# Optimization experiments

Hardware: AMD Instinct MI355X
Metric: run time of the kernel (lower is better)

The kernel has to match this reference:

```python
import jax, jax.numpy as jnp
import numpy as np

N, E, D, H, O = 10000, 640000, 128, 256, 1


def setup_inputs() -> dict:
    key = jax.random.key(0)
    ks = jax.random.split(key, 10)
    s = 0.05
    return {
        "x": jax.random.normal(ks[0], (N, D), dtype=jnp.float32),
        "edge_index": jax.random.randint(ks[1], (2, E), 0, N, dtype=jnp.int64),
        # GraphConv (PyG): lin_rel (with bias) applied to sum-aggregated neighbors,
        # lin_root (no bias) applied to self features.
        "W_rel": jax.random.normal(ks[2], (D, D), dtype=jnp.float32) * s,
        "b_rel": jnp.zeros((D,), dtype=jnp.float32),
        "W_root": jax.random.normal(ks[3], (D, D), dtype=jnp.float32) * s,
        # MLP: D -> H -> H -> O, ReLU between layers
        "W1": jax.random.normal(ks[4], (H, D), dtype=jnp.float32) * s,
        "b1": jnp.zeros((H,), dtype=jnp.float32),
        "W2": jax.random.normal(ks[5], (H, H), dtype=jnp.float32) * s,
        "b2": jnp.zeros((H,), dtype=jnp.float32),
        "W3": jax.random.normal(ks[6], (O, H), dtype=jnp.float32) * s,
        "b3": jnp.zeros((O,), dtype=jnp.float32),
    }


def reference(x, edge_index, W_rel, b_rel, W_root, W1, b1, W2, b2, W3, b3):
    src, dst = edge_index[0], edge_index[1]
    # gather source features along edges, scatter-add to destinations
    agg = jax.ops.segment_sum(x[src], dst, num_segments=N)  # [N, D]
    h = agg @ W_rel.T + b_rel + x @ W_root.T                 # GraphConv out [N, D]
    h = jax.nn.relu(h @ W1.T + b1)
    h = jax.nn.relu(h @ W2.T + b2)
    h = h @ W3.T + b3                                        # [N, O]
    return jax.nn.sigmoid(h)
```

## Files before the change

kernel.cpp:

```cpp
#include <hip/hip_runtime.h>
#include <hip/hip_bf16.h>
#include <cmath>

constexpr int N_NODES = 10000;
constexpr int D_IN = 128;
constexpr int H_DIM = 256;

constexpr int NB = 157;
constexpr int BCAP = 8192;
constexpr int EPB_A = 4096;

typedef unsigned short u16;
typedef short bf16x8 __attribute__((ext_vector_type(8)));
typedef float f32x4 __attribute__((ext_vector_type(4)));

__device__ inline u16 f2bf(float f) {
    return __builtin_bit_cast(u16, __float2bfloat16(f));
}
__device__ inline float bf2f(u16 u) {
    unsigned int v = (unsigned int)u << 16;
    return __builtin_bit_cast(float, v);
}

constexpr int PREP_XB = 1250, PREP_WB = 128;
__global__ __launch_bounds__(256)
void prep_kernel(const float* __restrict__ x,
                 const float* __restrict__ W_rel, const float* __restrict__ W_root,
                 const float* __restrict__ W1, const float* __restrict__ W2,
                 u16* __restrict__ x_bf,
                 u16* __restrict__ Wcat, u16* __restrict__ W1b, u16* __restrict__ W2b,
                 int* __restrict__ gcnt) {
    const int bid = blockIdx.x, t = threadIdx.x;
    if (bid < PREP_XB) {
        int idx = bid * 256 + t;
        if (idx >= N_NODES * 32) return;
        int row = idx >> 5, c = (idx & 31) * 4;
        float4 v = *reinterpret_cast<const float4*>(x + (size_t)row * D_IN + c);
        ushort4 o;
        o.x = f2bf(v.x); o.y = f2bf(v.y); o.z = f2bf(v.z); o.w = f2bf(v.w);
        *reinterpret_cast<ushort4*>(x_bf + (size_t)row * D_IN + c) = o;
    } else if (bid < PREP_XB + PREP_WB) {
        int idx4 = ((bid - PREP_XB) * 256 + t) * 4;
        const float* src;
        u16* dst;
        if (idx4 < 32768) {
            int n = idx4 >> 8, k = idx4 & 255;
            src = (k < 128) ? W_rel + n * 128 + k : W_root + n * 128 + (k - 128);
            dst = Wcat + idx4;
        } else if (idx4 < 65536) {
            src = W1 + (idx4 - 32768);
            dst = W1b + (idx4 - 32768);
        } else {
            src = W2 + (idx4 - 65536);
            dst = W2b + (idx4 - 65536);
        }
        float4 v = *reinterpret_cast<const float4*>(src);
        ushort4 o;
        o.x = f2bf(v.x); o.y = f2bf(v.y); o.z = f2bf(v.z); o.w = f2bf(v.w);
        *reinterpret_cast<ushort4*>(dst) = o;
    } else {
        if (t < NB) gcnt[t] = 0;
    }
}

__global__ __launch_bounds__(256)
void binsort_a(const int* __restrict__ ei, int* __restrict__ gcnt,
               int* __restrict__ buckets, int E) {
    __shared__ int lcnt[NB], gbase[NB];
    const int t = threadIdx.x;
    for (int i = t; i < NB; i += 256) lcnt[i] = 0;
    __syncthreads();
    const int e0 = blockIdx.x * EPB_A + t;
    int packed[16], lpos[16], bb[16];
#pragma unroll
    for (int j = 0; j < 16; ++j) {
        int e = e0 + j * 256;
        if (e < E) {
            int s = ei[e], d = ei[E + e];
            int b = d >> 6;
            bb[j] = b;
            packed[j] = ((d & 63) << 16) | s;
            lpos[j] = atomicAdd(&lcnt[b], 1);
        } else bb[j] = -1;
    }
    __syncthreads();
    for (int i = t; i < NB; i += 256)
        gbase[i] = atomicAdd(&gcnt[i], lcnt[i]);
    __syncthreads();
#pragma unroll
    for (int j = 0; j < 16; ++j)
        if (bb[j] >= 0)
            buckets[bb[j] * BCAP + gbase[bb[j]] + lpos[j]] = packed[j];
}

__global__ __launch_bounds__(512)
void mega_kernel(const int* __restrict__ gcnt, const int* __restrict__ buckets,
                 const u16* __restrict__ x_bf,
                 const u16* __restrict__ Wcat, const u16* __restrict__ W1b,
                 const u16* __restrict__ W2b,
                 const float* __restrict__ b_rel, const float* __restrict__ b1,
                 const float* __restrict__ b2, const float* __restrict__ W3,
                 const float* __restrict__ b3, float* __restrict__ out, int M) {
    __shared__ int edges[BCAP];
    __shared__ u16 ssrc[BCAP];
    __shared__ u16 bufA[64 * 264];
    __shared__ u16 bufH0[64 * 136];
    __shared__ int deg[64], cur[64], sbeg[64];
    __shared__ float part[64][4];
    const int b = blockIdx.x, t = threadIdx.x;
    const int w = t >> 6, lane = t & 63;
    const int wm = w >> 2, wn = w & 3;
    const int l16 = lane & 15, q = lane >> 4;
    const int r0 = b * 64;

    if (t < 64) deg[t] = 0;
    __syncthreads();
    int cnt = gcnt[b]; if (cnt > BCAP) cnt = BCAP;
    for (int i = t; i < cnt; i += 512) {
        int p = buckets[b * BCAP + i];
        edges[i] = p;
        atomicAdd(&deg[p >> 16], 1);
    }
    __syncthreads();
    if (t < 64) {
        int d = deg[t];
        int incl = d;
#pragma unroll
        for (int off = 1; off < 64; off <<= 1) {
            int o = __shfl_up(incl, off);
            if (t >= off) incl += o;
        }
        int excl = incl - d;
        cur[t] = excl;
        sbeg[t] = excl;
    }
    __syncthreads();
    for (int i = t; i < cnt; i += 512) {
        int p = edges[i];
        int pos = atomicAdd(&cur[p >> 16], 1);
        ssrc[pos] = (u16)(p & 0xffff);
    }
    for (int idx = t; idx < 64 * 16; idx += 512) {
        int row = idx >> 4, kc = (idx & 15) * 8;
        int gr = r0 + row; if (gr >= M) gr = M - 1;
        bf16x8 v = *reinterpret_cast<const bf16x8*>(x_bf + (size_t)gr * D_IN + kc);
        *reinterpret_cast<bf16x8*>(&bufA[row * 264 + 128 + kc]) = v;
    }
    __syncthreads();
    {
        const int c = (lane & 31) * 4;
        const int r = lane >> 5;
        for (int j = 0; j < 8; ++j) {
            int ln = w * 8 + j;
            int beg = sbeg[ln], dg = deg[ln];
            int half = (dg + 1) >> 1;
            int i = beg + (r ? half : 0);
            const int i1 = r ? beg + dg : beg + half;
            float4 a0 = {0, 0, 0, 0}, a1 = {0, 0, 0, 0};
            float4 a2 = {0, 0, 0, 0}, a3 = {0, 0, 0, 0};
            for (; i + 4 <= i1; i += 4) {
                int s0 = ssrc[i + 0], s1 = ssrc[i + 1];
                int s2 = ssrc[i + 2], s3 = ssrc[i + 3];
                ushort4 v0 = *reinterpret_cast<const ushort4*>(x_bf + (size_t)s0 * D_IN + c);
                ushort4 v1 = *reinterpret_cast<const ushort4*>(x_bf + (size_t)s1 * D_IN + c);
                ushort4 v2 = *reinterpret_cast<const ushort4*>(x_bf + (size_t)s2 * D_IN + c);
                ushort4 v3 = *reinterpret_cast<const ushort4*>(x_bf + (size_t)s3 * D_IN + c);
                a0.x += bf2f(v0.x); a0.y += bf2f(v0.y); a0.z += bf2f(v0.z); a0.w += bf2f(v0.w);
                a1.x += bf2f(v1.x); a1.y += bf2f(v1.y); a1.z += bf2f(v1.z); a1.w += bf2f(v1.w);
                a2.x += bf2f(v2.x); a2.y += bf2f(v2.y); a2.z += bf2f(v2.z); a2.w += bf2f(v2.w);
                a3.x += bf2f(v3.x); a3.y += bf2f(v3.y); a3.z += bf2f(v3.z); a3.w += bf2f(v3.w);
            }
            for (; i < i1; ++i) {
                int s = ssrc[i];
                ushort4 v = *reinterpret_cast<const ushort4*>(x_bf + (size_t)s * D_IN + c);
                a0.x += bf2f(v.x); a0.y += bf2f(v.y); a0.z += bf2f(v.z); a0.w += bf2f(v.w);
            }
            a0.x += a1.x + a2.x + a3.x;
            a0.y += a1.y + a2.y + a3.y;
            a0.z += a1.z + a2.z + a3.z;
            a0.w += a1.w + a2.w + a3.w;
            a0.x += __shfl_xor(a0.x, 32);
            a0.y += __shfl_xor(a0.y, 32);
            a0.z += __shfl_xor(a0.z, 32);
            a0.w += __shfl_xor(a0.w, 32);
            if (r == 0) {
                ushort4 o;
                o.x = f2bf(a0.x); o.y = f2bf(a0.y); o.z = f2bf(a0.z); o.w = f2bf(a0.w);
                *reinterpret_cast<ushort4*>(&bufA[ln * 264 + c]) = o;
            }
        }
    }
    __syncthreads();

    {
        f32x4 acc[2][2] = {};
#pragma unroll
        for (int k0 = 0; k0 < 256; k0 += 32) {
            bf16x8 af[2];
#pragma unroll
            for (int i = 0; i < 2; ++i)
                af[i] = *reinterpret_cast<const bf16x8*>(
                    &bufA[(wm * 32 + i * 16 + l16) * 264 + k0 + q * 8]);
#pragma unroll
            for (int jj = 0; jj < 2; ++jj) {
                int col = wn * 32 + jj * 16 + l16;
                bf16x8 bv = *reinterpret_cast<const bf16x8*>(
                    Wcat + (size_t)col * 256 + k0 + q * 8);
                acc[0][jj] = __builtin_amdgcn_mfma_f32_16x16x32_bf16(af[0], bv, acc[0][jj], 0, 0, 0);
                acc[1][jj] = __builtin_amdgcn_mfma_f32_16x16x32_bf16(af[1], bv, acc[1][jj], 0, 0, 0);
            }
        }
#pragma unroll
        for (int i = 0; i < 2; ++i)
#pragma unroll
            for (int jj = 0; jj < 2; ++jj) {
                int col = wn * 32 + jj * 16 + l16;
                float bb = b_rel[col];
#pragma unroll
                for (int r = 0; r < 4; ++r) {
                    int row = wm * 32 + i * 16 + q * 4 + r;
                    bufH0[row * 136 + col] = f2bf(acc[i][jj][r] + bb);
                }
            }
    }
    __syncthreads();

    {
        f32x4 acc[2][4] = {};
#pragma unroll
        for (int k0 = 0; k0 < 128; k0 += 32) {
            bf16x8 af[2];
#pragma unroll
            for (int i = 0; i < 2; ++i)
                af[i] = *reinterpret_cast<const bf16x8*>(
                    &bufH0[(wm * 32 + i * 16 + l16) * 136 + k0 + q * 8]);
#pragma unroll
            for (int jj = 0; jj < 4; ++jj) {
                int col = wn * 64 + jj * 16 + l16;
                bf16x8 bv = *reinterpret_cast<const bf16x8*>(
                    W1b + (size_t)col * 128 + k0 + q * 8);
                acc[0][jj] = __builtin_amdgcn_mfma_f32_16x16x32_bf16(af[0], bv, acc[0][jj], 0, 0, 0);
                acc[1][jj] = __builtin_amdgcn_mfma_f32_16x16x32_bf16(af[1], bv, acc[1][jj], 0, 0, 0);
            }
        }
        __syncthreads();
#pragma unroll
        for (int i = 0; i < 2; ++i)
#pragma unroll
            for (int jj = 0; jj < 4; ++jj) {
                int col = wn * 64 + jj * 16 + l16;
                float bb = b1[col];
#pragma unroll
                for (int r = 0; r < 4; ++r) {
                    int row = wm * 32 + i * 16 + q * 4 + r;
                    bufA[row * 264 + col] = f2bf(fmaxf(acc[i][jj][r] + bb, 0.f));
                }
            }
    }
    __syncthreads();

    {
        f32x4 acc[2][4] = {};
#pragma unroll
        for (int k0 = 0; k0 < 256; k0 += 32) {
            bf16x8 af[2];
#pragma unroll
            for (int i = 0; i < 2; ++i)
                af[i] = *reinterpret_cast<const bf16x8*>(
                    &bufA[(wm * 32 + i * 16 + l16) * 264 + k0 + q * 8]);
#pragma unroll
            for (int jj = 0; jj < 4; ++jj) {
                int col = wn * 64 + jj * 16 + l16;
                bf16x8 bv = *reinterpret_cast<const bf16x8*>(
                    W2b + (size_t)col * 256 + k0 + q * 8);
                acc[0][jj] = __builtin_amdgcn_mfma_f32_16x16x32_bf16(af[0], bv, acc[0][jj], 0, 0, 0);
                acc[1][jj] = __builtin_amdgcn_mfma_f32_16x16x32_bf16(af[1], bv, acc[1][jj], 0, 0, 0);
            }
        }
        float s[2][4] = {};
#pragma unroll
        for (int jj = 0; jj < 4; ++jj) {
            int col = wn * 64 + jj * 16 + l16;
            float bb = b2[col], ww = W3[col];
#pragma unroll
            for (int i = 0; i < 2; ++i)
#pragma unroll
                for (int r = 0; r < 4; ++r)
                    s[i][r] = fmaf(fmaxf(acc[i][jj][r] + bb, 0.f), ww, s[i][r]);
        }
#pragma unroll
        for (int off = 1; off < 16; off <<= 1)
#pragma unroll
            for (int i = 0; i < 2; ++i)
#pragma unroll
                for (int r = 0; r < 4; ++r)
                    s[i][r] += __shfl_xor(s[i][r], off);
        if (l16 == 0)
#pragma unroll
            for (int i = 0; i < 2; ++i)
#pragma unroll
                for (int r = 0; r < 4; ++r)
                    part[wm * 32 + i * 16 + q * 4 + r][wn] = s[i][r];
    }
    __syncthreads();
    if (t < 64) {
        int node = r0 + t;
        if (node < M) {
            float v = part[t][0] + part[t][1] + part[t][2] + part[t][3] + b3[0];
            out[node] = 1.0f / (1.0f + expf(-v));
        }
    }
}

extern "C" void kernel_launch(void* const* d_in, const int* in_sizes, int n_in,
                              void* d_out, int out_size, void* d_ws, size_t ws_size,
                              hipStream_t stream) {
    const float* x      = (const float*)d_in[0];
    const int*   ei     = (const int*)d_in[1];
    const float* W_rel  = (const float*)d_in[2];
    const float* b_rel  = (const float*)d_in[3];
    const float* W_root = (const float*)d_in[4];
    const float* W1     = (const float*)d_in[5];
    const float* b1     = (const float*)d_in[6];
    const float* W2     = (const float*)d_in[7];
    const float* b2     = (const float*)d_in[8];
    const float* W3     = (const float*)d_in[9];
    const float* b3     = (const float*)d_in[10];
    float* out = (float*)d_out;
    const int E = in_sizes[1] / 2;

    char* p = (char*)d_ws;
    auto carve = [&](size_t bytes) { char* r = p; p += (bytes + 63) & ~size_t(63); return r; };
    u16* x_bf = (u16*)carve((size_t)N_NODES * D_IN * 2);
    u16* Wcat = (u16*)carve(128 * 256 * 2);
    u16* W1b  = (u16*)carve(256 * 128 * 2);
    u16* W2b  = (u16*)carve(256 * 256 * 2);
    int* gcnt    = (int*)carve(NB * 4);
    int* buckets = (int*)carve((size_t)NB * BCAP * 4);

    prep_kernel<<<PREP_XB + PREP_WB + 1, 256, 0, stream>>>(
        x, W_rel, W_root, W1, W2, x_bf, Wcat, W1b, W2b, gcnt);
    binsort_a<<<(E + EPB_A - 1) / EPB_A, 256, 0, stream>>>(ei, gcnt, buckets, E);
    mega_kernel<<<NB, 512, 0, stream>>>(gcnt, buckets, x_bf, Wcat, W1b, W2b,
                                        b_rel, b1, b2, W3, b3, out, N_NODES);
}
```

Before: 140.5 us.

## Split gather from MLP, halve bucket size, stage weights in LDS

Splits the single fused kernel into two. A sort-and-gather kernel uses 32-node buckets across 313 blocks and writes aggregated bf16 features to global memory. A separate fused MLP kernel then stages the weight matrices into shared memory, processing W2 in two halves, before running the MFMA layers. The aim is to double the number of blocks for the latency-bound gather and to replace repeated global weight reads with LDS reads. The cost is an extra kernel launch, an agg buffer round trip through memory, and a smaller bucket capacity (3072) that could overflow on skewed in-degree graphs.

```diff
diff --git a/kernel.cpp b/kernel.cpp
--- a/kernel.cpp
+++ b/kernel.cpp
@@ -6,9 +6,9 @@
 constexpr int D_IN = 128;
 constexpr int H_DIM = 256;
 
-constexpr int NB = 157;
-constexpr int BCAP = 8192;
-constexpr int EPB_A = 4096;
+constexpr int NB = 313;
+constexpr int BCAP = 3072;
+constexpr int EPB_A = 2048;
 
 typedef unsigned short u16;
 typedef short bf16x8 __attribute__((ext_vector_type(8)));
@@ -59,7 +59,7 @@
         o.x = f2bf(v.x); o.y = f2bf(v.y); o.z = f2bf(v.z); o.w = f2bf(v.w);
         *reinterpret_cast<ushort4*>(dst) = o;
     } else {
-        if (t < NB) gcnt[t] = 0;
+        for (int i = t; i < NB; i += 256) gcnt[i] = 0;
     }
 }
 
@@ -71,15 +71,15 @@
     for (int i = t; i < NB; i += 256) lcnt[i] = 0;
     __syncthreads();
     const int e0 = blockIdx.x * EPB_A + t;
-    int packed[16], lpos[16], bb[16];
-#pragma unroll
-    for (int j = 0; j < 16; ++j) {
+    int packed[8], lpos[8], bb[8];
+#pragma unroll
+    for (int j = 0; j < 8; ++j) {
         int e = e0 + j * 256;
         if (e < E) {
             int s = ei[e], d = ei[E + e];
-            int b = d >> 6;
+            int b = d >> 5;
             bb[j] = b;
-            packed[j] = ((d & 63) << 16) | s;
+            packed[j] = ((d & 31) << 16) | s;
             lpos[j] = atomicAdd(&lcnt[b], 1);
         } else bb[j] = -1;
     }
@@ -88,32 +88,20 @@
         gbase[i] = atomicAdd(&gcnt[i], lcnt[i]);
     __syncthreads();
 #pragma unroll
-    for (int j = 0; j < 16; ++j)
+    for (int j = 0; j < 8; ++j)
         if (bb[j] >= 0)
             buckets[bb[j] * BCAP + gbase[bb[j]] + lpos[j]] = packed[j];
 }
 
 __global__ __launch_bounds__(512)
-void mega_kernel(const int* __restrict__ gcnt, const int* __restrict__ buckets,
-                 const u16* __restrict__ x_bf,
-                 const u16* __restrict__ Wcat, const u16* __restrict__ W1b,
-                 const u16* __restrict__ W2b,
-                 const float* __restrict__ b_rel, const float* __restrict__ b1,
-                 const float* __restrict__ b2, const float* __restrict__ W3,
-                 const float* __restrict__ b3, float* __restrict__ out, int M) {
+void sortgather(const int* __restrict__ gcnt, const int* __restrict__ buckets,
+                const u16* __restrict__ x_bf, u16* __restrict__ agg_bf, int M) {
     __shared__ int edges[BCAP];
     __shared__ u16 ssrc[BCAP];
-    __shared__ u16 bufA[64 * 264];
-    __shared__ u16 bufH0[64 * 136];
-    __shared__ int deg[64], cur[64], sbeg[64];
-    __shared__ float part[64][4];
+    __shared__ int deg[32], cur[32], sbeg[32];
     const int b = blockIdx.x, t = threadIdx.x;
     const int w = t >> 6, lane = t & 63;
-    const int wm = w >> 2, wn = w & 3;
-    const int l16 = lane & 15, q = lane >> 4;
-    const int r0 = b * 64;
-
-    if (t < 64) deg[t] = 0;
+    if (t < 32) deg[t] = 0;
     __syncthreads();
     int cnt = gcnt[b]; if (cnt > BCAP) cnt = BCAP;
     for (int i = t; i < cnt; i += 512) {
@@ -122,11 +110,11 @@
         atomicAdd(&deg[p >> 16], 1);
     }
     __syncthreads();
-    if (t < 64) {
+    if (t < 32) {
         int d = deg[t];
         int incl = d;
 #pragma unroll
-        for (int off = 1; off < 64; off <<= 1) {
+        for (int off = 1; off < 32; off <<= 1) {
             int o = __shfl_up(incl, off);
             if (t >= off) incl += o;
         }
@@ -140,55 +128,81 @@
         int pos = atomicAdd(&cur[p >> 16], 1);
         ssrc[pos] = (u16)(p & 0xffff);
     }
+    __syncthreads();
+    const int c = (lane & 31) * 4;
+    const int r = lane >> 5;
+#pragma unroll
+    for (int j = 0; j < 4; ++j) {
+        int ln = w * 4 + j;
+        int beg = sbeg[ln], dg = deg[ln];
+        int half = (dg + 1) >> 1;
+        int i = beg + (r ? half : 0);
+        const int i1 = r ? beg + dg : beg + half;
+        float4 a0 = {0, 0, 0, 0}, a1 = {0, 0, 0, 0};
+        float4 a2 = {0, 0, 0, 0}, a3 = {0, 0, 0, 0};
+        for (; i + 4 <= i1; i += 4) {
+            int s0 = ssrc[i + 0], s1 = ssrc[i + 1];
+            int s2 = ssrc[i + 2], s3 = ssrc[i + 3];
+            ushort4 v0 = *reinterpret_cast<const ushort4*>(x_bf + (size_t)s0 * D_IN + c);
+            ushort4 v1 = *reinterpret_cast<const ushort4*>(x_bf + (size_t)s1 * D_IN + c);
+            ushort4 v2 = *reinterpret_cast<const ushort4*>(x_bf + (size_t)s2 * D_IN + c);
+            ushort4 v3 = *reinterpret_cast<const ushort4*>(x_bf + (size_t)s3 * D_IN + c);
+            a0.x += bf2f(v0.x); a0.y += bf2f(v0.y); a0.z += bf2f(v0.z); a0.w += bf2f(v0.w);
+            a1.x += bf2f(v1.x); a1.y += bf2f(v1.y); a1.z += bf2f(v1.z); a1.w += bf2f(v1.w);
+            a2.x += bf2f(v2.x); a2.y += bf2f(v2.y); a2.z += bf2f(v2.z); a2.w += bf2f(v2.w);
+            a3.x += bf2f(v3.x); a3.y += bf2f(v3.y); a3.z += bf2f(v3.z); a3.w += bf2f(v3.w);
+        }
+        for (; i < i1; ++i) {
+            int s = ssrc[i];
+            ushort4 v = *reinterpret_cast<const ushort4*>(x_bf + (size_t)s * D_IN + c);
+            a0.x += bf2f(v.x); a0.y += bf2f(v.y); a0.z += bf2f(v.z); a0.w += bf2f(v.w);
+        }
+        a0.x += a1.x + a2.x + a3.x;
+        a0.y += a1.y + a2.y + a3.y;
+        a0.z += a1.z + a2.z + a3.z;
+        a0.w += a1.w + a2.w + a3.w;
+        a0.x += __shfl_xor(a0.x, 32);
+        a0.y += __shfl_xor(a0.y, 32);
+        a0.z += __shfl_xor(a0.z, 32);
+        a0.w += __shfl_xor(a0.w, 32);
+        int node = b * 32 + ln;
+        if (r == 0 && node < M) {
+            ushort4 o;
+            o.x = f2bf(a0.x); o.y = f2bf(a0.y); o.z = f2bf(a0.z); o.w = f2bf(a0.w);
+            *reinterpret_cast<ushort4*>(agg_bf + (size_t)node * D_IN + c) = o;
+        }
+    }
+}
+
+__global__ __launch_bounds__(512)
+void fused_mlp(const u16* __restrict__ agg_bf, const u16* __restrict__ x_bf,
+               const u16* __restrict__ Wcat, const u16* __restrict__ W1b,
+               const u16* __restrict__ W2b,
+               const float* __restrict__ b_rel, const float* __restrict__ b1,
+               const float* __restrict__ b2, const float* __restrict__ W3,
+               const float* __restrict__ b3, float* __restrict__ out, int M) {
+    __shared__ u16 bufA[64 * 264];
+    __shared__ u16 bufH0[64 * 136];
+    __shared__ u16 wbuf[34816];
+    __shared__ float part[64][4];
+    const int t = threadIdx.x, b = blockIdx.x;
+    const int w = t >> 6, lane = t & 63;
+    const int wm = w >> 2, wn = w & 3;
+    const int l16 = lane & 15, q = lane >> 4;
+    const int r0 = b * 64;
+
     for (int idx = t; idx < 64 * 16; idx += 512) {
         int row = idx >> 4, kc = (idx & 15) * 8;
         int gr = r0 + row; if (gr >= M) gr = M - 1;
-        bf16x8 v = *reinterpret_cast<const bf16x8*>(x_bf + (size_t)gr * D_IN + kc);
-        *reinterpret_cast<bf16x8*>(&bufA[row * 264 + 128 + kc]) = v;
-    }
-    __syncthreads();
-    {
-        const int c = (lane & 31) * 4;
-        const int r = lane >> 5;
-        for (int j = 0; j < 8; ++j) {
-            int ln = w * 8 + j;
-            int beg = sbeg[ln], dg = deg[ln];
-            int half = (dg + 1) >> 1;
-            int i = beg + (r ? half : 0);
-            const int i1 = r ? beg + dg : beg + half;
-            float4 a0 = {0, 0, 0, 0}, a1 = {0, 0, 0, 0};
-            float4 a2 = {0, 0, 0, 0}, a3 = {0, 0, 0, 0};
-            for (; i + 4 <= i1; i += 4) {
-                int s0 = ssrc[i + 0], s1 = ssrc[i + 1];
-                int s2 = ssrc[i + 2], s3 = ssrc[i + 3];
-                ushort4 v0 = *reinterpret_cast<const ushort4*>(x_bf + (size_t)s0 * D_IN + c);
-                ushort4 v1 = *reinterpret_cast<const ushort4*>(x_bf + (size_t)s1 * D_IN + c);
-                ushort4 v2 = *reinterpret_cast<const ushort4*>(x_bf + (size_t)s2 * D_IN + c);
-                ushort4 v3 = *reinterpret_cast<const ushort4*>(x_bf + (size_t)s3 * D_IN + c);
-                a0.x += bf2f(v0.x); a0.y += bf2f(v0.y); a0.z += bf2f(v0.z); a0.w += bf2f(v0.w);
-                a1.x += bf2f(v1.x); a1.y += bf2f(v1.y); a1.z += bf2f(v1.z); a1.w += bf2f(v1.w);
-                a2.x += bf2f(v2.x); a2.y += bf2f(v2.y); a2.z += bf2f(v2.z); a2.w += bf2f(v2.w);
-                a3.x += bf2f(v3.x); a3.y += bf2f(v3.y); a3.z += bf2f(v3.z); a3.w += bf2f(v3.w);
-            }
-            for (; i < i1; ++i) {
-                int s = ssrc[i];
-                ushort4 v = *reinterpret_cast<const ushort4*>(x_bf + (size_t)s * D_IN + c);
-                a0.x += bf2f(v.x); a0.y += bf2f(v.y); a0.z += bf2f(v.z); a0.w += bf2f(v.w);
-            }
-            a0.x += a1.x + a2.x + a3.x;
-            a0.y += a1.y + a2.y + a3.y;
-            a0.z += a1.z + a2.z + a3.z;
-            a0.w += a1.w + a2.w + a3.w;
-            a0.x += __shfl_xor(a0.x, 32);
-            a0.y += __shfl_xor(a0.y, 32);
-            a0.z += __shfl_xor(a0.z, 32);
-            a0.w += __shfl_xor(a0.w, 32);
-            if (r == 0) {
-                ushort4 o;
-                o.x = f2bf(a0.x); o.y = f2bf(a0.y); o.z = f2bf(a0.z); o.w = f2bf(a0.w);
-                *reinterpret_cast<ushort4*>(&bufA[ln * 264 + c]) = o;
-            }
-        }
+        bf16x8 v = *reinterpret_cast<const bf16x8*>(agg_bf + (size_t)gr * D_IN + kc);
+        *reinterpret_cast<bf16x8*>(&bufA[row * 264 + kc]) = v;
+        bf16x8 vx = *reinterpret_cast<const bf16x8*>(x_bf + (size_t)gr * D_IN + kc);
+        *reinterpret_cast<bf16x8*>(&bufA[row * 264 + 128 + kc]) = vx;
+    }
+    for (int idx = t; idx < 128 * 32; idx += 512) {
+        int row = idx >> 5, kc = (idx & 31) * 8;
+        bf16x8 v = *reinterpret_cast<const bf16x8*>(Wcat + (size_t)row * 256 + kc);
+        *reinterpret_cast<bf16x8*>(&wbuf[row * 264 + kc]) = v;
     }
     __syncthreads();
 
@@ -205,7 +219,7 @@
             for (int jj = 0; jj < 2; ++jj) {
                 int col = wn * 32 + jj * 16 + l16;
                 bf16x8 bv = *reinterpret_cast<const bf16x8*>(
-                    Wcat + (size_t)col * 256 + k0 + q * 8);
+                    &wbuf[col * 264 + k0 + q * 8]);
                 acc[0][jj] = __builtin_amdgcn_mfma_f32_16x16x32_bf16(af[0], bv, acc[0][jj], 0, 0, 0);
                 acc[1][jj] = __builtin_amdgcn_mfma_f32_16x16x32_bf16(af[1], bv, acc[1][jj], 0, 0, 0);
             }
@@ -225,6 +239,13 @@
     }
     __syncthreads();
 
+    for (int idx = t; idx < 256 * 16; idx += 512) {
+        int row = idx >> 4, kc = (idx & 15) * 8;
+        bf16x8 v = *reinterpret_cast<const bf16x8*>(W1b + (size_t)row * 128 + kc);
+        *reinterpret_cast<bf16x8*>(&wbuf[row * 136 + kc]) = v;
+    }
+    __syncthreads();
+
     {
         f32x4 acc[2][4] = {};
 #pragma unroll
@@ -238,12 +259,11 @@
             for (int jj = 0; jj < 4; ++jj) {
                 int col = wn * 64 + jj * 16 + l16;
                 bf16x8 bv = *reinterpret_cast<const bf16x8*>(
-                    W1b + (size_t)col * 128 + k0 + q * 8);
+                    &wbuf[col * 136 + k0 + q * 8]);
                 acc[0][jj] = __builtin_amdgcn_mfma_f32_16x16x32_bf16(af[0], bv, acc[0][jj], 0, 0, 0);
                 acc[1][jj] = __builtin_amdgcn_mfma_f32_16x16x32_bf16(af[1], bv, acc[1][jj], 0, 0, 0);
             }
         }
-        __syncthreads();
 #pragma unroll
         for (int i = 0; i < 2; ++i)
 #pragma unroll
@@ -257,10 +277,19 @@
                 }
             }
     }
-    __syncthreads();
-
-    {
-        f32x4 acc[2][4] = {};
+
+    float s[2][4] = {};
+#pragma unroll
+    for (int h = 0; h < 2; ++h) {
+        __syncthreads();
+        for (int idx = t; idx < 128 * 32; idx += 512) {
+            int row = idx >> 5, kc = (idx & 31) * 8;
+            bf16x8 v = *reinterpret_cast<const bf16x8*>(
+                W2b + (size_t)(h * 128 + row) * 256 + kc);
+            *reinterpret_cast<bf16x8*>(&wbuf[row * 264 + kc]) = v;
+        }
+        __syncthreads();
+        f32x4 acc[2][2] = {};
 #pragma unroll
         for (int k0 = 0; k0 < 256; k0 += 32) {
             bf16x8 af[2];
@@ -269,18 +298,17 @@
                 af[i] = *reinterpret_cast<const bf16x8*>(
                     &bufA[(wm * 32 + i * 16 + l16) * 264 + k0 + q * 8]);
 #pragma unroll
-            for (int jj = 0; jj < 4; ++jj) {
-                int col = wn * 64 + jj * 16 + l16;
+            for (int jj = 0; jj < 2; ++jj) {
+                int lcol = wn * 32 + jj * 16 + l16;
                 bf16x8 bv = *reinterpret_cast<const bf16x8*>(
-                    W2b + (size_t)col * 256 + k0 + q * 8);
+                    &wbuf[lcol * 264 + k0 + q * 8]);
                 acc[0][jj] = __builtin_amdgcn_mfma_f32_16x16x32_bf16(af[0], bv, acc[0][jj], 0, 0, 0);
                 acc[1][jj] = __builtin_amdgcn_mfma_f32_16x16x32_bf16(af[1], bv, acc[1][jj], 0, 0, 0);
             }
         }
-        float s[2][4] = {};
-#pragma unroll
-        for (int jj = 0; jj < 4; ++jj) {
-            int col = wn * 64 + jj * 16 + l16;
+#pragma unroll
+        for (int jj = 0; jj < 2; ++jj) {
+            int col = h * 128 + wn * 32 + jj * 16 + l16;
             float bb = b2[col], ww = W3[col];
 #pragma unroll
             for (int i = 0; i < 2; ++i)
@@ -288,20 +316,20 @@
                 for (int r = 0; r < 4; ++r)
                     s[i][r] = fmaf(fmaxf(acc[i][jj][r] + bb, 0.f), ww, s[i][r]);
         }
-#pragma unroll
-        for (int off = 1; off < 16; off <<= 1)
-#pragma unroll
-            for (int i = 0; i < 2; ++i)
-#pragma unroll
-                for (int r = 0; r < 4; ++r)
-                    s[i][r] += __shfl_xor(s[i][r], off);
-        if (l16 == 0)
-#pragma unroll
-            for (int i = 0; i < 2; ++i)
-#pragma unroll
-                for (int r = 0; r < 4; ++r)
-                    part[wm * 32 + i * 16 + q * 4 + r][wn] = s[i][r];
-    }
+    }
+#pragma unroll
+    for (int off = 1; off < 16; off <<= 1)
+#pragma unroll
+        for (int i = 0; i < 2; ++i)
+#pragma unroll
+            for (int r = 0; r < 4; ++r)
+                s[i][r] += __shfl_xor(s[i][r], off);
+    if (l16 == 0)
+#pragma unroll
+        for (int i = 0; i < 2; ++i)
+#pragma unroll
+            for (int r = 0; r < 4; ++r)
+                part[wm * 32 + i * 16 + q * 4 + r][wn] = s[i][r];
     __syncthreads();
     if (t < 64) {
         int node = r0 + t;
@@ -331,16 +359,18 @@
 
     char* p = (char*)d_ws;
     auto carve = [&](size_t bytes) { char* r = p; p += (bytes + 63) & ~size_t(63); return r; };
-    u16* x_bf = (u16*)carve((size_t)N_NODES * D_IN * 2);
-    u16* Wcat = (u16*)carve(128 * 256 * 2);
-    u16* W1b  = (u16*)carve(256 * 128 * 2);
-    u16* W2b  = (u16*)carve(256 * 256 * 2);
+    u16* x_bf   = (u16*)carve((size_t)N_NODES * D_IN * 2);
+    u16* agg_bf = (u16*)carve((size_t)N_NODES * D_IN * 2);
+    u16* Wcat   = (u16*)carve(128 * 256 * 2);
+    u16* W1b    = (u16*)carve(256 * 128 * 2);
+    u16* W2b    = (u16*)carve(256 * 256 * 2);
     int* gcnt    = (int*)carve(NB * 4);
     int* buckets = (int*)carve((size_t)NB * BCAP * 4);
 
     prep_kernel<<<PREP_XB + PREP_WB + 1, 256, 0, stream>>>(
         x, W_rel, W_root, W1, W2, x_bf, Wcat, W1b, W2b, gcnt);
     binsort_a<<<(E + EPB_A - 1) / EPB_A, 256, 0, stream>>>(ei, gcnt, buckets, E);
-    mega_kernel<<<NB, 512, 0, stream>>>(gcnt, buckets, x_bf, Wcat, W1b, W2b,
-                                        b_rel, b1, b2, W3, b3, out, N_NODES);
-}
+    sortgather<<<NB, 512, 0, stream>>>(gcnt, buckets, x_bf, agg_bf, N_NODES);
+    fused_mlp<<<(N_NODES + 63) / 64, 512, 0, stream>>>(
+        agg_bf, x_bf, Wcat, W1b, W2b, b_rel, b1, b2, W3, b3, out, N_NODES);
+}
```

After: 126.9 us. 1.11x faster.
